# Kernel optimization log

Hardware: AMD Instinct MI355X
Metric: run time of the kernel (lower is better)

Reference implementation:

```python
import jax, jax.numpy as jnp
import numpy as np

B, T, D, M = 4, 4096, 2048, 512


def setup_inputs() -> dict:
    key = jax.random.key(0)
    ks = jax.random.split(key, 6)
    x = jax.random.normal(ks[0], (B, T, D), dtype=jnp.float32)
    memory_state = jnp.zeros((B, M), dtype=jnp.float32)
    # xavier_normal-style init for the linear layers, zero biases
    Wv = jax.random.normal(ks[1], (M, D), dtype=jnp.float32) * np.float32(np.sqrt(2.0 / (D + M)))
    bv = jnp.zeros((M,), dtype=jnp.float32)
    Wg = jax.random.normal(ks[2], (D, D + M), dtype=jnp.float32) * np.float32(np.sqrt(2.0 / (2 * D + M)))
    bg = jnp.zeros((D,), dtype=jnp.float32)
    time_decay = jax.random.normal(ks[3], (M,), dtype=jnp.float32) * 0.01
    time_first = jax.random.normal(ks[4], (M,), dtype=jnp.float32) * 0.01
    return dict(x=x, memory_state=memory_state, Wv=Wv, bv=bv, Wg=Wg, bg=bg,
                time_decay=time_decay, time_first=time_first)


def reference(x, memory_state, Wv, bv, Wg, bg, time_decay, time_first):
    # v = value_proj(x): [B, T, M]
    v = jnp.einsum('btd,md->btm', x, Wv) + bv
    decay = jax.nn.sigmoid(time_decay) * 0.9 + 0.1   # [M]
    first = jax.nn.sigmoid(time_first)               # [M]

    # Recurrence: s_0 = memory_state; wv_t = v_t + s_t*first; s_{t+1} = s_t*decay + v_t
    def step(s, v_t):
        wv_t = v_t + s * first
        return s * decay + v_t, wv_t

    v_tb = jnp.swapaxes(v, 0, 1)                     # [T, B, M] for scan over time
    next_memory, wv_tb = jax.lax.scan(step, memory_state, v_tb)
    weighted_values = jnp.swapaxes(wv_tb, 0, 1)      # [B, T, M]

    # output = x + output_gate(concat[x, weighted_values])
    combined = jnp.concatenate([x, weighted_values], axis=-1)  # [B, T, D+M]
    output = x + jnp.einsum('btk,dk->btd', combined, Wg) + bg
    return output, next_memory
```

## Files before the change

kernel.cpp:

```cpp
#include <hip/hip_runtime.h>
#include <hip/hip_bf16.h>
#include <cstdint>
#include <cstddef>

#define B_DIM 4
#define T_DIM 4096
#define D_DIM 2048
#define M_DIM 512
#define NTOK  (B_DIM * T_DIM)
#define KCOMB (D_DIM + M_DIM)
#define NCHUNK 64
#define CLEN   64

typedef __attribute__((ext_vector_type(8)))  __bf16 bf16x8;
typedef __attribute__((ext_vector_type(16))) float  f32x16;
typedef __attribute__((ext_vector_type(4)))  float  f32x4;

__device__ __forceinline__ unsigned short f2bf(float f) {
  union { float f; unsigned u; } v; v.f = f;
  unsigned r = v.u + 0x7fffu + ((v.u >> 16) & 1u);
  return (unsigned short)(r >> 16);
}

__device__ __forceinline__ float bf2f(unsigned short u) {
  union { unsigned u; float f; } v; v.u = ((unsigned)u) << 16;
  return v.f;
}

__device__ __forceinline__ float sigmoidf(float x) { return 1.0f / (1.0f + expf(-x)); }

#define XBLK  ((NTOK * D_DIM / 4) / 256)
#define WVBLK ((M_DIM * D_DIM / 4) / 256)
#define WGBLK ((D_DIM * KCOMB / 4) / 256)
__global__ void cast_all_kernel(const float* __restrict__ x, const float* __restrict__ Wv,
                                const float* __restrict__ Wg,
                                unsigned short* __restrict__ comb,
                                unsigned short* __restrict__ WvB,
                                unsigned short* __restrict__ WgB) {
  int bid = blockIdx.x;
  const float* src; unsigned short* dst; size_t soff, doff;
  if (bid < XBLK) {
    int idx = bid * 256 + threadIdx.x;
    int n = idx >> 9;
    int c = (idx & 511) << 2;
    src = x;   soff = (size_t)n * D_DIM + c;
    dst = comb; doff = (size_t)n * KCOMB + c;
  } else if (bid < XBLK + WVBLK) {
    int idx = (bid - XBLK) * 256 + threadIdx.x;
    src = Wv;  soff = (size_t)idx * 4;
    dst = WvB; doff = (size_t)idx * 4;
  } else {
    int idx = (bid - XBLK - WVBLK) * 256 + threadIdx.x;
    src = Wg;  soff = (size_t)idx * 4;
    dst = WgB; doff = (size_t)idx * 4;
  }
  float4 v = *(const float4*)(src + soff);
  ushort4 o;
  o.x = f2bf(v.x); o.y = f2bf(v.y); o.z = f2bf(v.z); o.w = f2bf(v.w);
  *(ushort4*)(dst + doff) = o;
}

__global__ __launch_bounds__(M_DIM) void recur_partial(
    const float* __restrict__ v, const float* __restrict__ td, float* __restrict__ P) {
  int m = threadIdx.x;
  int b = blockIdx.x >> 6;
  int c = blockIdx.x & (NCHUNK - 1);
  float decay = sigmoidf(td[m]) * 0.9f + 0.1f;
  const float* vp = v + ((size_t)(b * T_DIM + c * CLEN)) * M_DIM + m;
  float p = 0.0f;
  for (int t0 = 0; t0 < CLEN; t0 += 8) {
    float vt[8];
#pragma unroll
    for (int u = 0; u < 8; ++u) vt[u] = vp[(size_t)(t0 + u) * M_DIM];
#pragma unroll
    for (int u = 0; u < 8; ++u) p = p * decay + vt[u];
  }
  P[(size_t)blockIdx.x * M_DIM + m] = p;
}

__global__ __launch_bounds__(M_DIM) void recur_apply(
    const float* __restrict__ v, const float* __restrict__ mem0,
    const float* __restrict__ td, const float* __restrict__ tf,
    const float* __restrict__ P,
    unsigned short* __restrict__ comb, float* __restrict__ nmem) {
  int m = threadIdx.x;
  int b = blockIdx.x >> 6;
  int c = blockIdx.x & (NCHUNK - 1);
  float decay = sigmoidf(td[m]) * 0.9f + 0.1f;
  float first = sigmoidf(tf[m]);
  float dL = decay;
  dL = dL * dL; dL = dL * dL; dL = dL * dL; dL = dL * dL; dL = dL * dL; dL = dL * dL;

  float s = mem0[b * M_DIM + m];
  const float* Pp = P + (size_t)(b * NCHUNK) * M_DIM + m;
  for (int ci = 0; ci < c; ++ci)
    s = s * dL + Pp[(size_t)ci * M_DIM];

  const float* vp = v + ((size_t)(b * T_DIM + c * CLEN)) * M_DIM + m;
  unsigned short* wp = comb + ((size_t)(b * T_DIM + c * CLEN)) * KCOMB + D_DIM + m;
  for (int t0 = 0; t0 < CLEN; t0 += 8) {
    float vt[8];
#pragma unroll
    for (int u = 0; u < 8; ++u) vt[u] = vp[(size_t)(t0 + u) * M_DIM];
#pragma unroll
    for (int u = 0; u < 8; ++u) {
      wp[(size_t)(t0 + u) * KCOMB] = f2bf(vt[u] + s * first);
      s = s * decay + vt[u];
    }
  }
  if (c == NCHUNK - 1) nmem[b * M_DIM + m] = s;
}

#define BM 128
#define BN 128
#define BK 64

template <bool ADD_X, int MODE>
__global__ __launch_bounds__(256) void gemm_bt(
    const unsigned short* __restrict__ A, int lda,
    const unsigned short* __restrict__ B, int ldb,
    const float* __restrict__ bias, const float* __restrict__ xadd,
    float* __restrict__ C, int N, int K) {
  const int tid = threadIdx.x;
  const int lane = tid & 63;
  const int wave = tid >> 6;
  const int wm = (wave >> 1) * 64;
  const int wn = (wave & 1) * 64;
  const int l31 = lane & 31;
  const int half = lane >> 5;

  int tileM, tileN;
  {
    int idx = blockIdx.x;
    int xcd = idx & 7, local = idx >> 3;
    if (MODE == 1) {
      tileN = (xcd * 2 + (local & 1)) * BN;
      tileM = (local >> 1) * BM;
    } else {
      tileM = (xcd * 16 + (local >> 2)) * BM;
      tileN = (local & 3) * BN;
    }
  }

  __shared__ unsigned short As[BM * BK];
  __shared__ unsigned short Bs[BN * BK];

  f32x16 acc[2][2] = {};

  for (int k0 = 0; k0 < K; k0 += BK) {
#pragma unroll
    for (int j = 0; j < 4; ++j) {
      int c = j * 256 + tid;
      int row = c >> 3;
      int kc = c & 7;
      int gkc = kc ^ (row & 7);
      const unsigned short* gA = A + (size_t)(tileM + row) * lda + k0 + gkc * 8;
      const unsigned short* gB = B + (size_t)(tileN + row) * ldb + k0 + gkc * 8;
      __builtin_amdgcn_global_load_lds((const __attribute__((address_space(1))) void*)gA,
                                       (__attribute__((address_space(3))) void*)(As + c * 8),
                                       16, 0, 0);
      __builtin_amdgcn_global_load_lds((const __attribute__((address_space(1))) void*)gB,
                                       (__attribute__((address_space(3))) void*)(Bs + c * 8),
                                       16, 0, 0);
    }
    __syncthreads();

#pragma unroll
    for (int s = 0; s < 4; ++s) {
      const int g = s * 2 + half;
      bf16x8 af[2], bfr[2];
#pragma unroll
      for (int i = 0; i < 2; ++i) {
        int ra = wm + i * 32 + l31;
        int rb = wn + i * 32 + l31;
        af[i]  = *(const bf16x8*)(As + ra * BK + ((g ^ (ra & 7)) * 8));
        bfr[i] = *(const bf16x8*)(Bs + rb * BK + ((g ^ (rb & 7)) * 8));
      }
#pragma unroll
      for (int mi = 0; mi < 2; ++mi)
#pragma unroll
        for (int ni = 0; ni < 2; ++ni)
          acc[mi][ni] = __builtin_amdgcn_mfma_f32_32x32x16_bf16(af[mi], bfr[ni], acc[mi][ni], 0, 0, 0);
    }
    __syncthreads();
  }

#pragma unroll
  for (int mi = 0; mi < 2; ++mi) {
#pragma unroll
    for (int ni = 0; ni < 2; ++ni) {
      int col = tileN + wn + ni * 32 + l31;
      float bcol = bias[col];
#pragma unroll
      for (int r = 0; r < 16; ++r) {
        int row = tileM + wm + mi * 32 + 4 * half + (r & 3) + 8 * (r >> 2);
        float val = acc[mi][ni][r] + bcol;
        if (ADD_X) val += xadd[(size_t)row * N + col];
        C[(size_t)row * N + col] = val;
      }
    }
  }
}

#define BAR_FENCE() do { asm volatile("" ::: "memory"); \
  __builtin_amdgcn_s_barrier(); asm volatile("" ::: "memory"); } while (0)

template <bool ADD_X, int LDA, int LDB, int NOUT, int KTOT>
__global__ __launch_bounds__(512, 2) void gemm256_bt(
    const unsigned short* __restrict__ Amat,
    const unsigned short* __restrict__ Bmat,
    const float* __restrict__ bias,
    const unsigned short* __restrict__ xadd,
    float* __restrict__ C) {
  constexpr int NK  = KTOT / 64;
  constexpr int NI  = NK / 2;
  constexpr int NTN = NOUT / 256;
  constexpr int NWG = (NTOK / 256) * NTN;
  constexpr int PERX = NWG / 8;

  __shared__ unsigned short As[2][256 * 64];
  __shared__ unsigned short Bs[2][256 * 64];

  const int tid  = threadIdx.x;
  const int lane = tid & 63;
  const int l15  = lane & 15;
  const int g4   = lane >> 4;
  const int wave = tid >> 6;
  const int wrow = (wave >> 2) * 128;
  const int wcol = (wave & 3) * 64;

  const int bid   = blockIdx.x;
  const int wgid  = (bid & 7) * PERX + (bid >> 3);
  const int tileM = (wgid / NTN) * 256;
  const int tileN = (wgid % NTN) * 256;

  const int row_lo = tid >> 3;
  const int scol   = (((tid & 7) ^ (row_lo & 7)) << 3);
  const unsigned short* pA = Amat + (size_t)(tileM + row_lo) * LDA + scol;
  const unsigned short* pB = Bmat + (size_t)(tileN + row_lo) * LDB + scol;

#define GSTAGE_A(b, h, kt) do { \
  _Pragma("unroll") for (int j = 0; j < 2; ++j) { \
    const unsigned short* _s = pA + (size_t)((h) * 128 + j * 64) * LDA + (kt) * 64; \
    __builtin_amdgcn_global_load_lds((const __attribute__((address_space(1))) void*)_s, \
        (__attribute__((address_space(3))) void*)(&As[(b)][(h) * 8192 + (j * 512 + tid) * 8]), \
        16, 0, 0); \
  } \
} while (0)

#define GSTAGE_B(b, h, kt) do { \
  _Pragma("unroll") for (int j = 0; j < 2; ++j) { \
    const unsigned short* _s = pB + (size_t)((h) * 128 + j * 64) * LDB + (kt) * 64; \
    __builtin_amdgcn_global_load_lds((const __attribute__((address_space(1))) void*)_s, \
        (__attribute__((address_space(3))) void*)(&Bs[(b)][(h) * 8192 + (j * 512 + tid) * 8]), \
        16, 0, 0); \
  } \
} while (0)

  f32x4  acc[8][4] = {};
  bf16x8 af[4][2];
  bf16x8 bf[2][2];
  bf16x8 bg[2][2];

#define GREAD_A(b, mh) do { \
  _Pragma("unroll") for (int mt = 0; mt < 4; ++mt) { \
    const int _r = wrow + (mh) * 64 + mt * 16 + l15; \
    _Pragma("unroll") for (int ks = 0; ks < 2; ++ks) \
      af[mt][ks] = *(const bf16x8*)(&As[(b)][_r * 64 + (((ks * 4 + g4) ^ (_r & 7)) << 3)]); \
  } \
} while (0)

#define GREAD_B(b, nh, dst) do { \
  _Pragma("unroll") for (int nt = 0; nt < 2; ++nt) { \
    const int _r = wcol + (nh) * 32 + nt * 16 + l15; \
    _Pragma("unroll") for (int ks = 0; ks < 2; ++ks) \
      dst[nt][ks] = *(const bf16x8*)(&Bs[(b)][_r * 64 + (((ks * 4 + g4) ^ (_r & 7)) << 3)]); \
  } \
} while (0)

#define GMFMA_Q(mh, nh, breg) do { \
  _Pragma("unroll") for (int ks = 0; ks < 2; ++ks) \
    _Pragma("unroll") for (int mt = 0; mt < 4; ++mt) \
      _Pragma("unroll") for (int nt = 0; nt < 2; ++nt) \
        acc[(mh) * 4 + mt][(nh) * 2 + nt] = __builtin_amdgcn_mfma_f32_16x16x32_bf16( \
            af[mt][ks], breg[nt][ks], acc[(mh) * 4 + mt][(nh) * 2 + nt], 0, 0, 0); \
} while (0)

#define GTAIL(mh, nh, breg) do { \
  BAR_FENCE(); \
  __builtin_amdgcn_s_setprio(1); \
  GMFMA_Q(mh, nh, breg); \
  __builtin_amdgcn_s_setprio(0); \
  BAR_FENCE(); \
} while (0)

  GSTAGE_A(0, 0, 0); GSTAGE_A(0, 1, 0);
  GSTAGE_B(0, 0, 0); GSTAGE_B(0, 1, 0);
  GSTAGE_A(1, 0, 1); GSTAGE_A(1, 1, 1);
  asm volatile("s_waitcnt vmcnt(4)" ::: "memory");
  BAR_FENCE();

#define GITER(i2, FULL) do { \
   \
  GREAD_A(0, 0); GREAD_B(0, 0, bf); \
  GSTAGE_B(1, 0, (i2) + 1); GSTAGE_B(1, 1, (i2) + 1); \
  GTAIL(0, 0, bf); \
   \
  GREAD_B(0, 1, bg); \
  GTAIL(0, 1, bg); \
   \
  GREAD_A(0, 1); \
  GTAIL(1, 1, bg); \
   \
  if (FULL) { GSTAGE_A(0, 0, (i2) + 2); GSTAGE_A(0, 1, (i2) + 2); \
              asm volatile("s_waitcnt vmcnt(4)" ::: "memory"); } \
  else      { asm volatile("s_waitcnt vmcnt(0)" ::: "memory"); } \
  GTAIL(1, 0, bf); \
   \
  GREAD_A(1, 0); GREAD_B(1, 0, bf); \
  if (FULL) { GSTAGE_B(0, 0, (i2) + 2); GSTAGE_B(0, 1, (i2) + 2); } \
  GTAIL(0, 0, bf); \
   \
  GREAD_B(1, 1, bg); \
  GTAIL(0, 1, bg); \
   \
  GREAD_A(1, 1); \
  GTAIL(1, 1, bg); \
   \
  if (FULL) { GSTAGE_A(1, 0, (i2) + 3); GSTAGE_A(1, 1, (i2) + 3); \
              asm volatile("s_waitcnt vmcnt(4)" ::: "memory"); } \
  GTAIL(1, 0, bf); \
} while (0)

#pragma unroll 1
  for (int i = 0; i < NI - 1; ++i) GITER(2 * i, 1);
  GITER(2 * (NI - 1), 0);

#undef GITER
#undef GTAIL
#undef GMFMA_Q
#undef GREAD_B
#undef GREAD_A
#undef GSTAGE_B
#undef GSTAGE_A

#pragma unroll
  for (int mt = 0; mt < 8; ++mt) {
#pragma unroll
    for (int nt = 0; nt < 4; ++nt) {
      const int col = tileN + wcol + nt * 16 + l15;
      const float bc = bias[col];
#pragma unroll
      for (int r = 0; r < 4; ++r) {
        const int row = tileM + wrow + mt * 16 + g4 * 4 + r;
        float val = acc[mt][nt][r] + bc;
        if (ADD_X) val += bf2f(xadd[(size_t)row * LDA + col]);
        C[(size_t)row * NOUT + col] = val;
      }
    }
  }
}

extern "C" void kernel_launch(void* const* d_in, const int* in_sizes, int n_in,
                              void* d_out, int out_size, void* d_ws, size_t ws_size,
                              hipStream_t stream) {
  const float* x   = (const float*)d_in[0];
  const float* mem = (const float*)d_in[1];
  const float* Wv  = (const float*)d_in[2];
  const float* bv  = (const float*)d_in[3];
  const float* Wg  = (const float*)d_in[4];
  const float* bg  = (const float*)d_in[5];
  const float* td  = (const float*)d_in[6];
  const float* tf  = (const float*)d_in[7];
  float* out = (float*)d_out;

  char* ws = (char*)d_ws;
  unsigned short* comb = (unsigned short*)ws;
  float* v = (float*)(ws + (size_t)NTOK * KCOMB * 2);
  unsigned short* WvB = (unsigned short*)((char*)v + (size_t)NTOK * M_DIM * 4);
  unsigned short* WgB = (unsigned short*)((char*)WvB + (size_t)M_DIM * D_DIM * 2);
  float* P = (float*)WvB;

  cast_all_kernel<<<XBLK + WVBLK + WGBLK, 256, 0, stream>>>(x, Wv, Wg, comb, WvB, WgB);

  gemm_bt<false, 0><<<(NTOK / BM) * (M_DIM / BN), 256, 0, stream>>>(
      comb, KCOMB, WvB, D_DIM, bv, nullptr, v, M_DIM, D_DIM);

  recur_partial<<<B_DIM * NCHUNK, M_DIM, 0, stream>>>(v, td, P);
  recur_apply<<<B_DIM * NCHUNK, M_DIM, 0, stream>>>(
      v, mem, td, tf, P, comb, out + (size_t)NTOK * D_DIM);

  gemm256_bt<true, KCOMB, KCOMB, D_DIM, KCOMB>
      <<<(NTOK / 256) * (D_DIM / 256), 512, 0, stream>>>(comb, WgB, bg, comb, out);
}
```

Baseline: 478.8 us.

## Cut per-quadrant barriers in GEMM main loop and regroup global staging

```diff
diff --git a/kernel.cpp b/kernel.cpp
--- a/kernel.cpp
+++ b/kernel.cpp
@@ -279,19 +279,13 @@
 } while (0)
 
 #define GMFMA_Q(mh, nh, breg) do { \
+  __builtin_amdgcn_s_setprio(1); \
   _Pragma("unroll") for (int ks = 0; ks < 2; ++ks) \
     _Pragma("unroll") for (int mt = 0; mt < 4; ++mt) \
       _Pragma("unroll") for (int nt = 0; nt < 2; ++nt) \
         acc[(mh) * 4 + mt][(nh) * 2 + nt] = __builtin_amdgcn_mfma_f32_16x16x32_bf16( \
             af[mt][ks], breg[nt][ks], acc[(mh) * 4 + mt][(nh) * 2 + nt], 0, 0, 0); \
-} while (0)
-
-#define GTAIL(mh, nh, breg) do { \
-  BAR_FENCE(); \
-  __builtin_amdgcn_s_setprio(1); \
-  GMFMA_Q(mh, nh, breg); \
   __builtin_amdgcn_s_setprio(0); \
-  BAR_FENCE(); \
 } while (0)
 
   GSTAGE_A(0, 0, 0); GSTAGE_A(0, 1, 0);
@@ -302,34 +296,32 @@
 
 #define GITER(i2, FULL) do { \
    \
+  GSTAGE_B(1, 0, (i2) + 1); GSTAGE_B(1, 1, (i2) + 1); \
   GREAD_A(0, 0); GREAD_B(0, 0, bf); \
-  GSTAGE_B(1, 0, (i2) + 1); GSTAGE_B(1, 1, (i2) + 1); \
-  GTAIL(0, 0, bf); \
-   \
+  GMFMA_Q(0, 0, bf); \
   GREAD_B(0, 1, bg); \
-  GTAIL(0, 1, bg); \
-   \
+  GMFMA_Q(0, 1, bg); \
   GREAD_A(0, 1); \
-  GTAIL(1, 1, bg); \
-   \
+  GMFMA_Q(1, 1, bg); \
+  BAR_FENCE();   \
   if (FULL) { GSTAGE_A(0, 0, (i2) + 2); GSTAGE_A(0, 1, (i2) + 2); \
-              asm volatile("s_waitcnt vmcnt(4)" ::: "memory"); } \
-  else      { asm volatile("s_waitcnt vmcnt(0)" ::: "memory"); } \
-  GTAIL(1, 0, bf); \
+              GSTAGE_B(0, 0, (i2) + 2); GSTAGE_B(0, 1, (i2) + 2); } \
+  GMFMA_Q(1, 0, bf);   \
+  if (FULL) asm volatile("s_waitcnt vmcnt(8)" ::: "memory"); \
+  else      asm volatile("s_waitcnt vmcnt(0)" ::: "memory"); \
+  BAR_FENCE();   \
    \
   GREAD_A(1, 0); GREAD_B(1, 0, bf); \
-  if (FULL) { GSTAGE_B(0, 0, (i2) + 2); GSTAGE_B(0, 1, (i2) + 2); } \
-  GTAIL(0, 0, bf); \
-   \
+  GMFMA_Q(0, 0, bf); \
   GREAD_B(1, 1, bg); \
-  GTAIL(0, 1, bg); \
-   \
+  GMFMA_Q(0, 1, bg); \
   GREAD_A(1, 1); \
-  GTAIL(1, 1, bg); \
-   \
-  if (FULL) { GSTAGE_A(1, 0, (i2) + 3); GSTAGE_A(1, 1, (i2) + 3); \
-              asm volatile("s_waitcnt vmcnt(4)" ::: "memory"); } \
-  GTAIL(1, 0, bf); \
+  GMFMA_Q(1, 1, bg); \
+  BAR_FENCE();   \
+  if (FULL) { GSTAGE_A(1, 0, (i2) + 3); GSTAGE_A(1, 1, (i2) + 3); } \
+  GMFMA_Q(1, 0, bf); \
+  if (FULL) { asm volatile("s_waitcnt vmcnt(4)" ::: "memory"); \
+              BAR_FENCE(); }   \
 } while (0)
 
 #pragma unroll 1
@@ -337,7 +329,6 @@
   GITER(2 * (NI - 1), 0);
 
 #undef GITER
-#undef GTAIL
 #undef GMFMA_Q
 #undef GREAD_B
 #undef GREAD_A
```

Result: no change. 473.0 us (-1.2%).
